# Optimization experiments

Hardware: AMD Instinct MI355X
Metric: run time of the kernel (lower is better)

The kernel has to match this reference:

```python
import jax, jax.numpy as jnp
import numpy as np

B, T, S = 4, 16, 4096
H, KV, D, DIM = 32, 8, 128, 4096
BASE = 10000.0
START = 2048
SCALE = 1.0 / np.sqrt(D)


def _rope(t, cos, sin):
    # t: [B, T, nh, D]; ggml 'normal' rope rotates adjacent pairs (x[2i], x[2i+1])
    b, tt, nh, d = t.shape
    t2 = t.reshape(b, tt, nh, d // 2, 2)
    x0, x1 = t2[..., 0], t2[..., 1]
    c = cos[None, :, None, :]  # [1, T, 1, D/2]
    s = sin[None, :, None, :]
    r = jnp.stack([x0 * c - x1 * s, x0 * s + x1 * c], axis=-1)
    return r.reshape(b, tt, nh, d)


def setup_inputs() -> dict:
    key = jax.random.key(0)
    ks = jax.random.split(key, 8)
    x = jax.random.normal(ks[0], (B, T, DIM), dtype=jnp.float32)
    k_cache = jax.random.normal(ks[1], (B, S, KV, D), dtype=jnp.float32)
    v_cache = jax.random.normal(ks[2], (B, S, KV, D), dtype=jnp.float32)
    wq = jax.random.normal(ks[3], (H * D, DIM), dtype=jnp.float32) * 0.02
    wk = jax.random.normal(ks[4], (KV * D, DIM), dtype=jnp.float32) * 0.02
    wv = jax.random.normal(ks[5], (KV * D, DIM), dtype=jnp.float32) * 0.02
    wo = jax.random.normal(ks[6], (DIM, H * D), dtype=jnp.float32) * 0.02
    input_pos = jnp.arange(T, dtype=jnp.int32) + START  # contiguous decode chunk
    inv_freq = BASE ** (-jnp.arange(0, D, 2, dtype=jnp.float32) / D)  # [D/2]
    ang = input_pos.astype(jnp.float32)[:, None] * inv_freq[None, :]  # [T, D/2]
    freqs_cos = jnp.cos(ang)
    freqs_sin = jnp.sin(ang)
    # causal mask: kv position <= query absolute position, [T, S] bool
    attn_mask = jnp.arange(S, dtype=jnp.int32)[None, :] <= input_pos[:, None]
    return {"x": x, "freqs_cos": freqs_cos, "freqs_sin": freqs_sin,
            "input_pos": input_pos, "attn_mask": attn_mask,
            "k_cache": k_cache, "v_cache": v_cache,
            "wq": wq, "wk": wk, "wv": wv, "wo": wo}


def reference(x, freqs_cos, freqs_sin, input_pos, attn_mask, k_cache, v_cache, wq, wk, wv, wo):
    b, t, _ = x.shape
    q = (x @ wq.T).reshape(b, t, H, D)
    k = (x @ wk.T).reshape(b, t, KV, D)
    v = (x @ wv.T).reshape(b, t, KV, D)
    q = _rope(q, freqs_cos, freqs_sin)
    k = _rope(k, freqs_cos, freqs_sin)
    # KV-cache scatter (index_copy_ along dim 1)
    kc = k_cache.at[:, input_pos].set(k)  # [B, S, KV, D]
    vc = v_cache.at[:, input_pos].set(v)
    g = H // KV
    qh = q.transpose(0, 2, 1, 3).reshape(b, KV, g, t, D)  # [B, KV, g, T, D]
    kf = kc.transpose(0, 2, 1, 3)  # [B, KV, S, D]
    vf = vc.transpose(0, 2, 1, 3)
    scores = jnp.einsum('bkgtd,bksd->bkgts', qh, kf) * SCALE
    scores = jnp.where(attn_mask[None, None, None], scores, jnp.finfo(scores.dtype).min)
    probs = jax.nn.softmax(scores, axis=-1)
    y = jnp.einsum('bkgts,bksd->bkgtd', probs, vf)  # [B, KV, g, T, D]
    y = y.reshape(b, H, t, D).transpose(0, 2, 1, 3).reshape(b, t, H * D)
    return y @ wo.T
```

## Files before the change

kernel.cpp:

```cpp
#include <hip/hip_runtime.h>


#define SCALE_F 0.08838834764831845f

typedef __attribute__((ext_vector_type(8))) short bf16x8;
typedef __attribute__((ext_vector_type(4))) float f32x4;

__device__ __forceinline__ unsigned short f2b(float f) {
    union { float f; unsigned u; } v; v.f = f;
    unsigned r = v.u + 0x7FFFu + ((v.u >> 16) & 1u);
    return (unsigned short)(r >> 16);
}

__device__ __forceinline__ bf16x8 pack8(float4 a, float4 b) {
    bf16x8 r;
    r[0] = (short)f2b(a.x); r[1] = (short)f2b(a.y); r[2] = (short)f2b(a.z); r[3] = (short)f2b(a.w);
    r[4] = (short)f2b(b.x); r[5] = (short)f2b(b.y); r[6] = (short)f2b(b.z); r[7] = (short)f2b(b.w);
    return r;
}

__global__ __launch_bounds__(256) void qkv_gemm_kernel(
    const float* __restrict__ x,
    const float* __restrict__ wq, const float* __restrict__ wk, const float* __restrict__ wvp,
    float* __restrict__ part)
{
    __shared__ unsigned short x_lds[64][72];
    __shared__ unsigned short w_lds[32][72];
    const int tid = threadIdx.x, lane = tid & 63, wid = tid >> 6;
    const int n0 = blockIdx.x * 32;
    const int split = blockIdx.y;
    const int k_base = split * 512;

    const float* wptr; int nn;
    if (n0 < 4096)      { wptr = wq;  nn = n0; }
    else if (n0 < 5120) { wptr = wk;  nn = n0 - 4096; }
    else                { wptr = wvp; nn = n0 - 5120; }

    const int xr = tid >> 2, xc = (tid & 3) * 16;
    const int wr = tid >> 3, wc = (tid & 7) * 8;
    const float* xp = x + xr * 4096 + k_base + xc;
    const float* wp = wptr + (nn + wr) * 4096 + k_base + wc;

    float4 rx0, rx1, rx2, rx3, rw0, rw1;
#define LOADQ(IT) do { const float* xq_ = xp + (IT) * 64; const float* wq_ = wp + (IT) * 64; \
    rx0 = *(const float4*)(xq_);      rx1 = *(const float4*)(xq_ + 4);  \
    rx2 = *(const float4*)(xq_ + 8);  rx3 = *(const float4*)(xq_ + 12); \
    rw0 = *(const float4*)(wq_);      rw1 = *(const float4*)(wq_ + 4); } while (0)

    f32x4 acc0 = {0.f,0.f,0.f,0.f}, acc1 = {0.f,0.f,0.f,0.f};
    LOADQ(0);
    for (int it = 0; it < 8; ++it) {
        *(bf16x8*)&x_lds[xr][xc]     = pack8(rx0, rx1);
        *(bf16x8*)&x_lds[xr][xc + 8] = pack8(rx2, rx3);
        *(bf16x8*)&w_lds[wr][wc]     = pack8(rw0, rw1);
        __syncthreads();
        if (it < 7) LOADQ(it + 1);
        #pragma unroll
        for (int kk = 0; kk < 2; ++kk) {
            bf16x8 a  = *(bf16x8*)&x_lds[16 * wid + (lane & 15)][kk * 32 + 8 * (lane >> 4)];
            bf16x8 b0 = *(bf16x8*)&w_lds[(lane & 15)][kk * 32 + 8 * (lane >> 4)];
            bf16x8 b1 = *(bf16x8*)&w_lds[16 + (lane & 15)][kk * 32 + 8 * (lane >> 4)];
            acc0 = __builtin_amdgcn_mfma_f32_16x16x32_bf16(a, b0, acc0, 0, 0, 0);
            acc1 = __builtin_amdgcn_mfma_f32_16x16x32_bf16(a, b1, acc1, 0, 0, 0);
        }
        __syncthreads();
    }
#undef LOADQ
    #pragma unroll
    for (int nt = 0; nt < 2; ++nt) {
        f32x4 acc = nt ? acc1 : acc0;
        #pragma unroll
        for (int r = 0; r < 4; ++r) {
            int row = 16 * wid + 4 * (lane >> 4) + r;
            part[(split * 64 + row) * 6144 + n0 + nt * 16 + (lane & 15)] = acc[r];
        }
    }
}

__global__ __launch_bounds__(256) void qkv_reduce_kernel(
    const float* __restrict__ part,
    const float* __restrict__ fcos, const float* __restrict__ fsin,
    unsigned short* __restrict__ q_out, unsigned short* __restrict__ k_new,
    unsigned short* __restrict__ v_new)
{
    const int gid = blockIdx.x * 256 + threadIdx.x;
    const int m = gid / 1536;
    const int n = (gid % 1536) * 4;
    float4 s = {0.f,0.f,0.f,0.f};
    #pragma unroll
    for (int sp = 0; sp < 8; ++sp) {
        float4 v = *(const float4*)(part + (size_t)(sp * 64 + m) * 6144 + n);
        s.x += v.x; s.y += v.y; s.z += v.z; s.w += v.w;
    }
    const int t = m & 15, b = m >> 4;
    ushort4 o;
    if (n < 5120) {
        int d = n & 127;
        float c0 = fcos[t * 64 + (d >> 1)],     s0 = fsin[t * 64 + (d >> 1)];
        float c1 = fcos[t * 64 + (d >> 1) + 1], s1 = fsin[t * 64 + (d >> 1) + 1];
        o.x = f2b(s.x * c0 - s.y * s0);
        o.y = f2b(s.x * s0 + s.y * c0);
        o.z = f2b(s.z * c1 - s.w * s1);
        o.w = f2b(s.z * s1 + s.w * c1);
    } else {
        o.x = f2b(s.x); o.y = f2b(s.y); o.z = f2b(s.z); o.w = f2b(s.w);
    }
    if (n < 4096) {
        int h = n >> 7, d = n & 127;
        int row = (b * 8 + (h >> 2)) * 64 + (h & 3) * 16 + t;
        *(ushort4*)(q_out + row * 128 + d) = o;
    } else if (n < 5120) {
        int idx = n - 4096, kvh = idx >> 7, d = idx & 127;
        *(ushort4*)(k_new + ((b * 8 + kvh) * 16 + t) * 128 + d) = o;
    } else {
        int idx = n - 5120, kvh = idx >> 7, d = idx & 127;
        *(ushort4*)(v_new + ((b * 8 + kvh) * 16 + t) * 128 + d) = o;
    }
}

__global__ __launch_bounds__(256) void attn_kernel(
    const float* __restrict__ k_cache, const float* __restrict__ v_cache,
    const unsigned short* __restrict__ q_glob,
    const unsigned short* __restrict__ k_new, const unsigned short* __restrict__ v_new,
    float* __restrict__ y_part, float* __restrict__ ml)
{
    __shared__ unsigned short smem[32256];
    unsigned short* kv_lds = smem;
    unsigned short* p_lds  = smem + 21504;

    const int bk = blockIdx.x >> 4;
    const int c  = blockIdx.x & 15;
    const int b = bk >> 3, kvh = bk & 7;
    const int tid = threadIdx.x, lane = tid & 63, wid = tid >> 6;
    const int s0 = c * 128;
    const bool last = (c == 15);

    bf16x8 aq[4];
    {
        const unsigned short* qp = q_glob + (bk * 64 + 16 * wid + (lane & 15)) * 128 + 8 * (lane >> 4);
        #pragma unroll
        for (int kk = 0; kk < 4; ++kk) aq[kk] = *(const bf16x8*)(qp + kk * 32);
    }

    const int rr = tid >> 5, ln4 = (tid & 31) * 4;
    {
        const float* kb = k_cache + ((size_t)(b * 4096 + s0) * 8 + kvh) * 128;
        #pragma unroll 4
        for (int it = 0; it < 16; ++it) {
            int srow = it * 8 + rr;
            float4 kf = *(const float4*)(kb + (size_t)srow * 1024 + ln4);
            ushort4 k4; k4.x = f2b(kf.x); k4.y = f2b(kf.y); k4.z = f2b(kf.z); k4.w = f2b(kf.w);
            *(ushort4*)&kv_lds[srow * 136 + ln4] = k4;
        }
        if (last) {
            int row = tid >> 4, c8 = (tid & 15) * 8;
            *(bf16x8*)&kv_lds[(128 + row) * 136 + c8] =
                *(const bf16x8*)(k_new + (bk * 16 + row) * 128 + c8);
        }
    }
    __syncthreads();

    f32x4 sc[9];
    f32x4 zero4 = {0.f,0.f,0.f,0.f};
    #pragma unroll
    for (int st = 0; st < 9; ++st) sc[st] = zero4;
    #pragma unroll
    for (int kk = 0; kk < 4; ++kk) {
        #pragma unroll
        for (int st = 0; st < 9; ++st) {
            if (st == 8 && !last) continue;
            bf16x8 bf = *(bf16x8*)&kv_lds[(st * 16 + (lane & 15)) * 136 + kk * 32 + 8 * (lane >> 4)];
            sc[st] = __builtin_amdgcn_mfma_f32_16x16x32_bf16(aq[kk], bf, sc[st], 0, 0, 0);
        }
    }

    float mrow[4], lrow[4];
    #pragma unroll
    for (int r = 0; r < 4; ++r) {
        int trow = 4 * (lane >> 4) + r;
        float mx = -3.0e38f;
        #pragma unroll
        for (int st = 0; st < 9; ++st) {
            if (st == 8 && !last) continue;
            float s = sc[st][r] * SCALE_F;
            if (st == 8 && (lane & 15) > trow) s = -3.0e38f;
            sc[st][r] = s;
            mx = fmaxf(mx, s);
        }
        mx = fmaxf(mx, __shfl_xor(mx, 1));
        mx = fmaxf(mx, __shfl_xor(mx, 2));
        mx = fmaxf(mx, __shfl_xor(mx, 4));
        mx = fmaxf(mx, __shfl_xor(mx, 8));
        float sum = 0.f;
        #pragma unroll
        for (int st = 0; st < 9; ++st) {
            if (st == 8 && !last) continue;
            float p = __expf(sc[st][r] - mx);
            sc[st][r] = p;
            sum += p;
        }
        sum += __shfl_xor(sum, 1);
        sum += __shfl_xor(sum, 2);
        sum += __shfl_xor(sum, 4);
        sum += __shfl_xor(sum, 8);
        mrow[r] = mx; lrow[r] = sum;
    }

    #pragma unroll
    for (int st = 0; st < 9; ++st) {
        if (st == 8 && !last) continue;
        #pragma unroll
        for (int r = 0; r < 4; ++r)
            p_lds[(16 * wid + 4 * (lane >> 4) + r) * 168 + st * 16 + (lane & 15)] = f2b(sc[st][r]);
    }
    if ((lane & 15) == 0) {
        #pragma unroll
        for (int r = 0; r < 4; ++r) {
            int row = 16 * wid + 4 * (lane >> 4) + r;
            ml[(bk * 16 + c) * 128 + row * 2 + 0] = mrow[r];
            ml[(bk * 16 + c) * 128 + row * 2 + 1] = lrow[r];
        }
    }
    __syncthreads();

    {
        const float* vb = v_cache + ((size_t)(b * 4096 + s0) * 8 + kvh) * 128;
        #pragma unroll 4
        for (int it = 0; it < 16; ++it) {
            int srow = it * 8 + rr;
            float4 vf = *(const float4*)(vb + (size_t)srow * 1024 + ln4);
            kv_lds[(ln4 + 0) * 168 + srow] = f2b(vf.x);
            kv_lds[(ln4 + 1) * 168 + srow] = f2b(vf.y);
            kv_lds[(ln4 + 2) * 168 + srow] = f2b(vf.z);
            kv_lds[(ln4 + 3) * 168 + srow] = f2b(vf.w);
        }
        if (last) {
            int row = tid >> 4, c8 = (tid & 15) * 8;
            bf16x8 vv = *(const bf16x8*)(v_new + (bk * 16 + row) * 128 + c8);
            #pragma unroll
            for (int u = 0; u < 8; ++u)
                kv_lds[(c8 + u) * 168 + 128 + row] = (unsigned short)vv[u];
            int pr = tid >> 2, pc = (tid & 3) * 4;
            #pragma unroll
            for (int u = 0; u < 4; ++u) p_lds[pr * 168 + 144 + pc + u] = 0;
            int vr = tid >> 1, vc = (tid & 1) * 8;
            #pragma unroll
            for (int u = 0; u < 8; ++u) kv_lds[vr * 168 + 144 + vc + u] = 0;
        }
    }
    __syncthreads();

    f32x4 o_[8];
    #pragma unroll
    for (int nt = 0; nt < 8; ++nt) o_[nt] = zero4;
    #pragma unroll
    for (int ks = 0; ks < 5; ++ks) {
        if (ks == 4 && !last) continue;
        bf16x8 a = *(bf16x8*)&p_lds[(16 * wid + (lane & 15)) * 168 + ks * 32 + 8 * (lane >> 4)];
        #pragma unroll
        for (int nt = 0; nt < 8; ++nt) {
            bf16x8 bf = *(bf16x8*)&kv_lds[(nt * 16 + (lane & 15)) * 168 + ks * 32 + 8 * (lane >> 4)];
            o_[nt] = __builtin_amdgcn_mfma_f32_16x16x32_bf16(a, bf, o_[nt], 0, 0, 0);
        }
    }
    float* yp = y_part + (size_t)(bk * 16 + c) * 8192;
    #pragma unroll
    for (int nt = 0; nt < 8; ++nt) {
        #pragma unroll
        for (int r = 0; r < 4; ++r)
            yp[(16 * wid + 4 * (lane >> 4) + r) * 128 + nt * 16 + (lane & 15)] = o_[nt][r];
    }
}

__global__ __launch_bounds__(256) void combine_kernel(
    const float* __restrict__ y_part, const float* __restrict__ ml,
    unsigned short* __restrict__ y_attn)
{
    const int bid = blockIdx.x;
    const int bk = bid >> 3, rg = bid & 7;
    const int b = bk >> 3, kvh = bk & 7;
    const int tid = threadIdx.x;
    const int d = tid & 127, r2 = tid >> 7;
    for (int rr = 0; rr < 8; rr += 2) {
        int row = rg * 8 + rr + r2;
        float mv[16], lv[16], M = -3.0e38f;
        #pragma unroll
        for (int cc = 0; cc < 16; ++cc) {
            mv[cc] = ml[(bk * 16 + cc) * 128 + row * 2 + 0];
            lv[cc] = ml[(bk * 16 + cc) * 128 + row * 2 + 1];
            M = fmaxf(M, mv[cc]);
        }
        float den = 0.f, acc = 0.f;
        #pragma unroll
        for (int cc = 0; cc < 16; ++cc) {
            float co = __expf(mv[cc] - M);
            den += co * lv[cc];
            acc += co * y_part[((size_t)(bk * 16 + cc) * 64 + row) * 128 + d];
        }
        float y = acc / den;
        int gi = row >> 4, t = row & 15;
        y_attn[(b * 16 + t) * 4096 + (kvh * 4 + gi) * 128 + d] = f2b(y);
    }
}

__global__ __launch_bounds__(256) void proj_gemm_kernel(
    const unsigned short* __restrict__ y_attn, const float* __restrict__ wo,
    float* __restrict__ part)
{
    __shared__ unsigned short a_lds[64][72];
    __shared__ unsigned short w_lds[32][72];
    const int tid = threadIdx.x, lane = tid & 63, wid = tid >> 6;
    const int n0 = blockIdx.x * 32;
    const int k_base = blockIdx.y * 512;

    const int ar = tid >> 2, ac = (tid & 3) * 16;
    const int wr = tid >> 3, wc = (tid & 7) * 8;
    const unsigned short* ap = y_attn + ar * 4096 + k_base + ac;
    const float* wp = wo + (n0 + wr) * 4096 + k_base + wc;

    bf16x8 ra0, ra1; float4 rw0, rw1;
#define LOADP(IT) do { const unsigned short* aq_ = ap + (IT) * 64; const float* wq_ = wp + (IT) * 64; \
    ra0 = *(const bf16x8*)(aq_); ra1 = *(const bf16x8*)(aq_ + 8); \
    rw0 = *(const float4*)(wq_); rw1 = *(const float4*)(wq_ + 4); } while (0)

    f32x4 acc0 = {0.f,0.f,0.f,0.f}, acc1 = {0.f,0.f,0.f,0.f};
    LOADP(0);
    for (int it = 0; it < 8; ++it) {
        *(bf16x8*)&a_lds[ar][ac]     = ra0;
        *(bf16x8*)&a_lds[ar][ac + 8] = ra1;
        *(bf16x8*)&w_lds[wr][wc]     = pack8(rw0, rw1);
        __syncthreads();
        if (it < 7) LOADP(it + 1);
        #pragma unroll
        for (int kk = 0; kk < 2; ++kk) {
            bf16x8 a  = *(bf16x8*)&a_lds[16 * wid + (lane & 15)][kk * 32 + 8 * (lane >> 4)];
            bf16x8 b0 = *(bf16x8*)&w_lds[(lane & 15)][kk * 32 + 8 * (lane >> 4)];
            bf16x8 b1 = *(bf16x8*)&w_lds[16 + (lane & 15)][kk * 32 + 8 * (lane >> 4)];
            acc0 = __builtin_amdgcn_mfma_f32_16x16x32_bf16(a, b0, acc0, 0, 0, 0);
            acc1 = __builtin_amdgcn_mfma_f32_16x16x32_bf16(a, b1, acc1, 0, 0, 0);
        }
        __syncthreads();
    }
#undef LOADP
    #pragma unroll
    for (int nt = 0; nt < 2; ++nt) {
        f32x4 acc = nt ? acc1 : acc0;
        #pragma unroll
        for (int r = 0; r < 4; ++r) {
            int row = 16 * wid + 4 * (lane >> 4) + r;
            part[(size_t)(blockIdx.y * 64 + row) * 4096 + n0 + nt * 16 + (lane & 15)] = acc[r];
        }
    }
}

__global__ __launch_bounds__(256) void proj_reduce_kernel(
    const float* __restrict__ part, float* __restrict__ out)
{
    const int gid = blockIdx.x * 256 + threadIdx.x;
    const int m = gid >> 10;
    const int n = (gid & 1023) * 4;
    float4 s = {0.f,0.f,0.f,0.f};
    #pragma unroll
    for (int sp = 0; sp < 8; ++sp) {
        float4 v = *(const float4*)(part + (size_t)(sp * 64 + m) * 4096 + n);
        s.x += v.x; s.y += v.y; s.z += v.z; s.w += v.w;
    }
    *(float4*)(out + (size_t)m * 4096 + n) = s;
}

extern "C" void kernel_launch(void* const* d_in, const int* in_sizes, int n_in,
                              void* d_out, int out_size, void* d_ws, size_t ws_size,
                              hipStream_t stream)
{
    const float* x       = (const float*)d_in[0];
    const float* fcos    = (const float*)d_in[1];
    const float* fsin    = (const float*)d_in[2];
    const float* k_cache = (const float*)d_in[5];
    const float* v_cache = (const float*)d_in[6];
    const float* wq      = (const float*)d_in[7];
    const float* wk      = (const float*)d_in[8];
    const float* wv      = (const float*)d_in[9];
    const float* wo      = (const float*)d_in[10];

    char* p = (char*)d_ws;
    unsigned short* q_out  = (unsigned short*)p; p += 4 * 8 * 64 * 128 * 2;
    unsigned short* k_new  = (unsigned short*)p; p += 4 * 8 * 16 * 128 * 2;
    unsigned short* v_new  = (unsigned short*)p; p += 4 * 8 * 16 * 128 * 2;
    unsigned short* y_attn = (unsigned short*)p; p += 64 * 4096 * 2;
    float* mlbuf  = (float*)p; p += 32 * 16 * 64 * 2 * 4;
    float* y_part = (float*)p; p += (size_t)32 * 16 * 64 * 128 * 4;
    float* bigbuf = (float*)p;

    qkv_gemm_kernel<<<dim3(192, 8), 256, 0, stream>>>(x, wq, wk, wv, bigbuf);
    qkv_reduce_kernel<<<384, 256, 0, stream>>>(bigbuf, fcos, fsin, q_out, k_new, v_new);
    attn_kernel<<<512, 256, 0, stream>>>(k_cache, v_cache, q_out, k_new, v_new, y_part, mlbuf);
    combine_kernel<<<256, 256, 0, stream>>>(y_part, mlbuf, y_attn);
    proj_gemm_kernel<<<dim3(128, 8), 256, 0, stream>>>(y_attn, wo, bigbuf);
    proj_reduce_kernel<<<256, 256, 0, stream>>>(bigbuf, (float*)d_out);
}
```

Measured before the change: 78.50 us.

## Restructure QKV and output GEMMs to stage activations once and stream weights directly into MFMA registers

Both skinny GEMMs now load the whole 64x256 activation slice into LDS once per block. Each wave then streams its own 32 weight rows straight from global memory into registers, using double-buffered prefetch, and feeds them as MFMA B operands. This removes the per-iteration LDS round-trip and barriers for weights and reuses each weight fragment across four M tiles. The split-K factor doubles from 8 to 16, so the reduce kernels sum more partials and the partial buffers grow. Weight loads per lane are less coalesced (stride across rows), which may cost bandwidth on this weight-bound workload.

```diff
diff --git a/kernel.cpp b/kernel.cpp
--- a/kernel.cpp
+++ b/kernel.cpp
@@ -24,57 +24,67 @@
     const float* __restrict__ wq, const float* __restrict__ wk, const float* __restrict__ wvp,
     float* __restrict__ part)
 {
-    __shared__ unsigned short x_lds[64][72];
-    __shared__ unsigned short w_lds[32][72];
+    __shared__ unsigned short a_lds[64][258];
     const int tid = threadIdx.x, lane = tid & 63, wid = tid >> 6;
-    const int n0 = blockIdx.x * 32;
-    const int split = blockIdx.y;
-    const int k_base = split * 512;
-
+    const int k_base = blockIdx.y * 256;
+
+    {
+        const int sr = tid >> 2, sq = tid & 3;
+        const float* xp = x + (size_t)sr * 4096 + k_base;
+        #pragma unroll
+        for (int j = 0; j < 8; ++j) {
+            int col = 32 * j + 8 * sq;
+            float4 p0 = *(const float4*)(xp + col);
+            float4 p1 = *(const float4*)(xp + col + 4);
+            *(bf16x8*)&a_lds[sr][col] = pack8(p0, p1);
+        }
+    }
+    __syncthreads();
+
+    const int n0 = blockIdx.x * 128 + wid * 32;
     const float* wptr; int nn;
     if (n0 < 4096)      { wptr = wq;  nn = n0; }
     else if (n0 < 5120) { wptr = wk;  nn = n0 - 4096; }
     else                { wptr = wvp; nn = n0 - 5120; }
 
-    const int xr = tid >> 2, xc = (tid & 3) * 16;
-    const int wr = tid >> 3, wc = (tid & 7) * 8;
-    const float* xp = x + xr * 4096 + k_base + xc;
-    const float* wp = wptr + (nn + wr) * 4096 + k_base + wc;
-
-    float4 rx0, rx1, rx2, rx3, rw0, rw1;
-#define LOADQ(IT) do { const float* xq_ = xp + (IT) * 64; const float* wq_ = wp + (IT) * 64; \
-    rx0 = *(const float4*)(xq_);      rx1 = *(const float4*)(xq_ + 4);  \
-    rx2 = *(const float4*)(xq_ + 8);  rx3 = *(const float4*)(xq_ + 12); \
-    rw0 = *(const float4*)(wq_);      rw1 = *(const float4*)(wq_ + 4); } while (0)
-
-    f32x4 acc0 = {0.f,0.f,0.f,0.f}, acc1 = {0.f,0.f,0.f,0.f};
-    LOADQ(0);
-    for (int it = 0; it < 8; ++it) {
-        *(bf16x8*)&x_lds[xr][xc]     = pack8(rx0, rx1);
-        *(bf16x8*)&x_lds[xr][xc + 8] = pack8(rx2, rx3);
-        *(bf16x8*)&w_lds[wr][wc]     = pack8(rw0, rw1);
-        __syncthreads();
-        if (it < 7) LOADQ(it + 1);
-        #pragma unroll
-        for (int kk = 0; kk < 2; ++kk) {
-            bf16x8 a  = *(bf16x8*)&x_lds[16 * wid + (lane & 15)][kk * 32 + 8 * (lane >> 4)];
-            bf16x8 b0 = *(bf16x8*)&w_lds[(lane & 15)][kk * 32 + 8 * (lane >> 4)];
-            bf16x8 b1 = *(bf16x8*)&w_lds[16 + (lane & 15)][kk * 32 + 8 * (lane >> 4)];
-            acc0 = __builtin_amdgcn_mfma_f32_16x16x32_bf16(a, b0, acc0, 0, 0, 0);
-            acc1 = __builtin_amdgcn_mfma_f32_16x16x32_bf16(a, b1, acc1, 0, 0, 0);
-        }
-        __syncthreads();
-    }
-#undef LOADQ
-    #pragma unroll
-    for (int nt = 0; nt < 2; ++nt) {
-        f32x4 acc = nt ? acc1 : acc0;
-        #pragma unroll
-        for (int r = 0; r < 4; ++r) {
-            int row = 16 * wid + 4 * (lane >> 4) + r;
-            part[(split * 64 + row) * 6144 + n0 + nt * 16 + (lane & 15)] = acc[r];
-        }
-    }
+    const int l15 = lane & 15, lh = lane >> 4;
+    const float* w0 = wptr + (size_t)(nn + l15) * 4096 + k_base + 8 * lh;
+    const float* w1 = w0 + 16 * 4096;
+
+    float4 buf0[4], buf1[4];
+#define ISSUE0(S) do { buf0[0]=*(const float4*)(w0+(S)*32); buf0[1]=*(const float4*)(w0+(S)*32+4); \
+                       buf0[2]=*(const float4*)(w1+(S)*32); buf0[3]=*(const float4*)(w1+(S)*32+4); } while(0)
+#define ISSUE1(S) do { buf1[0]=*(const float4*)(w0+(S)*32); buf1[1]=*(const float4*)(w0+(S)*32+4); \
+                       buf1[2]=*(const float4*)(w1+(S)*32); buf1[3]=*(const float4*)(w1+(S)*32+4); } while(0)
+
+    f32x4 acc[4][2];
+    #pragma unroll
+    for (int m = 0; m < 4; ++m) { acc[m][0] = (f32x4){0,0,0,0}; acc[m][1] = (f32x4){0,0,0,0}; }
+
+    ISSUE0(0); ISSUE1(1);
+    #pragma unroll
+    for (int s = 0; s < 8; ++s) {
+        bf16x8 b0, b1;
+        if ((s & 1) == 0) { b0 = pack8(buf0[0], buf0[1]); b1 = pack8(buf0[2], buf0[3]); if (s < 6) ISSUE0(s + 2); }
+        else              { b0 = pack8(buf1[0], buf1[1]); b1 = pack8(buf1[2], buf1[3]); if (s < 6) ISSUE1(s + 2); }
+        #pragma unroll
+        for (int m = 0; m < 4; ++m) {
+            bf16x8 a = *(bf16x8*)&a_lds[16 * m + l15][s * 32 + 8 * lh];
+            acc[m][0] = __builtin_amdgcn_mfma_f32_16x16x32_bf16(a, b0, acc[m][0], 0, 0, 0);
+            acc[m][1] = __builtin_amdgcn_mfma_f32_16x16x32_bf16(a, b1, acc[m][1], 0, 0, 0);
+        }
+    }
+#undef ISSUE0
+#undef ISSUE1
+
+    float* pp = part + (size_t)blockIdx.y * 64 * 6144;
+    #pragma unroll
+    for (int m = 0; m < 4; ++m)
+        #pragma unroll
+        for (int nh = 0; nh < 2; ++nh)
+            #pragma unroll
+            for (int r = 0; r < 4; ++r)
+                pp[(16 * m + 4 * lh + r) * 6144 + n0 + nh * 16 + l15] = acc[m][nh][r];
 }
 
 __global__ __launch_bounds__(256) void qkv_reduce_kernel(
@@ -88,7 +98,7 @@
     const int n = (gid % 1536) * 4;
     float4 s = {0.f,0.f,0.f,0.f};
     #pragma unroll
-    for (int sp = 0; sp < 8; ++sp) {
+    for (int sp = 0; sp < 16; ++sp) {
         float4 v = *(const float4*)(part + (size_t)(sp * 64 + m) * 6144 + n);
         s.x += v.x; s.y += v.y; s.z += v.z; s.w += v.w;
     }
@@ -307,50 +317,60 @@
     const unsigned short* __restrict__ y_attn, const float* __restrict__ wo,
     float* __restrict__ part)
 {
-    __shared__ unsigned short a_lds[64][72];
-    __shared__ unsigned short w_lds[32][72];
+    __shared__ unsigned short a_lds[64][258];
     const int tid = threadIdx.x, lane = tid & 63, wid = tid >> 6;
-    const int n0 = blockIdx.x * 32;
-    const int k_base = blockIdx.y * 512;
-
-    const int ar = tid >> 2, ac = (tid & 3) * 16;
-    const int wr = tid >> 3, wc = (tid & 7) * 8;
-    const unsigned short* ap = y_attn + ar * 4096 + k_base + ac;
-    const float* wp = wo + (n0 + wr) * 4096 + k_base + wc;
-
-    bf16x8 ra0, ra1; float4 rw0, rw1;
-#define LOADP(IT) do { const unsigned short* aq_ = ap + (IT) * 64; const float* wq_ = wp + (IT) * 64; \
-    ra0 = *(const bf16x8*)(aq_); ra1 = *(const bf16x8*)(aq_ + 8); \
-    rw0 = *(const float4*)(wq_); rw1 = *(const float4*)(wq_ + 4); } while (0)
-
-    f32x4 acc0 = {0.f,0.f,0.f,0.f}, acc1 = {0.f,0.f,0.f,0.f};
-    LOADP(0);
-    for (int it = 0; it < 8; ++it) {
-        *(bf16x8*)&a_lds[ar][ac]     = ra0;
-        *(bf16x8*)&a_lds[ar][ac + 8] = ra1;
-        *(bf16x8*)&w_lds[wr][wc]     = pack8(rw0, rw1);
-        __syncthreads();
-        if (it < 7) LOADP(it + 1);
-        #pragma unroll
-        for (int kk = 0; kk < 2; ++kk) {
-            bf16x8 a  = *(bf16x8*)&a_lds[16 * wid + (lane & 15)][kk * 32 + 8 * (lane >> 4)];
-            bf16x8 b0 = *(bf16x8*)&w_lds[(lane & 15)][kk * 32 + 8 * (lane >> 4)];
-            bf16x8 b1 = *(bf16x8*)&w_lds[16 + (lane & 15)][kk * 32 + 8 * (lane >> 4)];
-            acc0 = __builtin_amdgcn_mfma_f32_16x16x32_bf16(a, b0, acc0, 0, 0, 0);
-            acc1 = __builtin_amdgcn_mfma_f32_16x16x32_bf16(a, b1, acc1, 0, 0, 0);
-        }
-        __syncthreads();
-    }
-#undef LOADP
-    #pragma unroll
-    for (int nt = 0; nt < 2; ++nt) {
-        f32x4 acc = nt ? acc1 : acc0;
-        #pragma unroll
-        for (int r = 0; r < 4; ++r) {
-            int row = 16 * wid + 4 * (lane >> 4) + r;
-            part[(size_t)(blockIdx.y * 64 + row) * 4096 + n0 + nt * 16 + (lane & 15)] = acc[r];
-        }
-    }
+    const int k_base = blockIdx.y * 256;
+
+    {
+        const int sr = tid >> 2, sq = tid & 3;
+        const unsigned short* ap = y_attn + (size_t)sr * 4096 + k_base;
+        #pragma unroll
+        for (int j = 0; j < 8; ++j) {
+            int col = 32 * j + 8 * sq;
+            *(bf16x8*)&a_lds[sr][col] = *(const bf16x8*)(ap + col);
+        }
+    }
+    __syncthreads();
+
+    const int n0 = blockIdx.x * 128 + wid * 32;
+    const int l15 = lane & 15, lh = lane >> 4;
+    const float* w0 = wo + (size_t)(n0 + l15) * 4096 + k_base + 8 * lh;
+    const float* w1 = w0 + 16 * 4096;
+
+    float4 buf0[4], buf1[4];
+#define ISSUE0(S) do { buf0[0]=*(const float4*)(w0+(S)*32); buf0[1]=*(const float4*)(w0+(S)*32+4); \
+                       buf0[2]=*(const float4*)(w1+(S)*32); buf0[3]=*(const float4*)(w1+(S)*32+4); } while(0)
+#define ISSUE1(S) do { buf1[0]=*(const float4*)(w0+(S)*32); buf1[1]=*(const float4*)(w0+(S)*32+4); \
+                       buf1[2]=*(const float4*)(w1+(S)*32); buf1[3]=*(const float4*)(w1+(S)*32+4); } while(0)
+
+    f32x4 acc[4][2];
+    #pragma unroll
+    for (int m = 0; m < 4; ++m) { acc[m][0] = (f32x4){0,0,0,0}; acc[m][1] = (f32x4){0,0,0,0}; }
+
+    ISSUE0(0); ISSUE1(1);
+    #pragma unroll
+    for (int s = 0; s < 8; ++s) {
+        bf16x8 b0, b1;
+        if ((s & 1) == 0) { b0 = pack8(buf0[0], buf0[1]); b1 = pack8(buf0[2], buf0[3]); if (s < 6) ISSUE0(s + 2); }
+        else              { b0 = pack8(buf1[0], buf1[1]); b1 = pack8(buf1[2], buf1[3]); if (s < 6) ISSUE1(s + 2); }
+        #pragma unroll
+        for (int m = 0; m < 4; ++m) {
+            bf16x8 a = *(bf16x8*)&a_lds[16 * m + l15][s * 32 + 8 * lh];
+            acc[m][0] = __builtin_amdgcn_mfma_f32_16x16x32_bf16(a, b0, acc[m][0], 0, 0, 0);
+            acc[m][1] = __builtin_amdgcn_mfma_f32_16x16x32_bf16(a, b1, acc[m][1], 0, 0, 0);
+        }
+    }
+#undef ISSUE0
+#undef ISSUE1
+
+    float* pp = part + (size_t)blockIdx.y * 64 * 4096;
+    #pragma unroll
+    for (int m = 0; m < 4; ++m)
+        #pragma unroll
+        for (int nh = 0; nh < 2; ++nh)
+            #pragma unroll
+            for (int r = 0; r < 4; ++r)
+                pp[(16 * m + 4 * lh + r) * 4096 + n0 + nh * 16 + l15] = acc[m][nh][r];
 }
 
 __global__ __launch_bounds__(256) void proj_reduce_kernel(
@@ -361,7 +381,7 @@
     const int n = (gid & 1023) * 4;
     float4 s = {0.f,0.f,0.f,0.f};
     #pragma unroll
-    for (int sp = 0; sp < 8; ++sp) {
+    for (int sp = 0; sp < 16; ++sp) {
         float4 v = *(const float4*)(part + (size_t)(sp * 64 + m) * 4096 + n);
         s.x += v.x; s.y += v.y; s.z += v.z; s.w += v.w;
     }
@@ -391,10 +411,10 @@
     float* y_part = (float*)p; p += (size_t)32 * 16 * 64 * 128 * 4;
     float* bigbuf = (float*)p;
 
-    qkv_gemm_kernel<<<dim3(192, 8), 256, 0, stream>>>(x, wq, wk, wv, bigbuf);
+    qkv_gemm_kernel<<<dim3(48, 16), 256, 0, stream>>>(x, wq, wk, wv, bigbuf);
     qkv_reduce_kernel<<<384, 256, 0, stream>>>(bigbuf, fcos, fsin, q_out, k_new, v_new);
     attn_kernel<<<512, 256, 0, stream>>>(k_cache, v_cache, q_out, k_new, v_new, y_part, mlbuf);
     combine_kernel<<<256, 256, 0, stream>>>(y_part, mlbuf, y_attn);
-    proj_gemm_kernel<<<dim3(128, 8), 256, 0, stream>>>(y_attn, wo, bigbuf);
+    proj_gemm_kernel<<<dim3(32, 16), 256, 0, stream>>>(y_attn, wo, bigbuf);
     proj_reduce_kernel<<<256, 256, 0, stream>>>(bigbuf, (float*)d_out);
 }
```

Result: slower. 80.70 us (+2.8%).

## Stage GEMM tiles via direct global-to-LDS loads with double buffering and wider N tiles

Applied to the files above, without the earlier changes.

Both the QKV and output-projection GEMMs now copy fp32 (and bf16) tiles straight from global memory into swizzled, double-buffered LDS using global_load_lds. Conversion to bf16 happens when fragments are read from LDS instead of before the store. Each block also covers 64 output columns instead of 32, halving the grid, and the bf16 rounding helper switches to the library intrinsic. The aim is to overlap weight streaming with MFMA work and cut register round-trips, at the cost of more LDS per block, fewer blocks, and repeated pack work on every fragment read.

```diff
diff --git a/kernel.cpp b/kernel.cpp
--- a/kernel.cpp
+++ b/kernel.cpp
@@ -1,4 +1,5 @@
 #include <hip/hip_runtime.h>
+#include <hip/hip_bf16.h>
 
 
 #define SCALE_F 0.08838834764831845f
@@ -7,9 +8,8 @@
 typedef __attribute__((ext_vector_type(4))) float f32x4;
 
 __device__ __forceinline__ unsigned short f2b(float f) {
-    union { float f; unsigned u; } v; v.f = f;
-    unsigned r = v.u + 0x7FFFu + ((v.u >> 16) & 1u);
-    return (unsigned short)(r >> 16);
+    __hip_bfloat16 h = __float2bfloat16(f);
+    return *reinterpret_cast<unsigned short*>(&h);
 }
 
 __device__ __forceinline__ bf16x8 pack8(float4 a, float4 b) {
@@ -19,62 +19,74 @@
     return r;
 }
 
+__device__ __forceinline__ void gl_lds16(const void* g, void* l) {
+    __builtin_amdgcn_global_load_lds(
+        (const __attribute__((address_space(1))) void*)g,
+        (__attribute__((address_space(3))) void*)l, 16, 0, 0);
+}
+
 __global__ __launch_bounds__(256) void qkv_gemm_kernel(
     const float* __restrict__ x,
     const float* __restrict__ wq, const float* __restrict__ wk, const float* __restrict__ wvp,
     float* __restrict__ part)
 {
-    __shared__ unsigned short x_lds[64][72];
-    __shared__ unsigned short w_lds[32][72];
+    __shared__ float lds[2][4096];
     const int tid = threadIdx.x, lane = tid & 63, wid = tid >> 6;
-    const int n0 = blockIdx.x * 32;
-    const int split = blockIdx.y;
-    const int k_base = split * 512;
+    const int l15 = lane & 15, lh = lane >> 4;
+    const int n0 = blockIdx.x * 64;
+    const int k_base = blockIdx.y * 512;
 
     const float* wptr; int nn;
     if (n0 < 4096)      { wptr = wq;  nn = n0; }
     else if (n0 < 5120) { wptr = wk;  nn = n0 - 4096; }
     else                { wptr = wvp; nn = n0 - 5120; }
 
-    const int xr = tid >> 2, xc = (tid & 3) * 16;
-    const int wr = tid >> 3, wc = (tid & 7) * 8;
-    const float* xp = x + xr * 4096 + k_base + xc;
-    const float* wp = wptr + (nn + wr) * 4096 + k_base + wc;
-
-    float4 rx0, rx1, rx2, rx3, rw0, rw1;
-#define LOADQ(IT) do { const float* xq_ = xp + (IT) * 64; const float* wq_ = wp + (IT) * 64; \
-    rx0 = *(const float4*)(xq_);      rx1 = *(const float4*)(xq_ + 4);  \
-    rx2 = *(const float4*)(xq_ + 8);  rx3 = *(const float4*)(xq_ + 12); \
-    rw0 = *(const float4*)(wq_);      rw1 = *(const float4*)(wq_ + 4); } while (0)
-
-    f32x4 acc0 = {0.f,0.f,0.f,0.f}, acc1 = {0.f,0.f,0.f,0.f};
-    LOADQ(0);
-    for (int it = 0; it < 8; ++it) {
-        *(bf16x8*)&x_lds[xr][xc]     = pack8(rx0, rx1);
-        *(bf16x8*)&x_lds[xr][xc + 8] = pack8(rx2, rx3);
-        *(bf16x8*)&w_lds[wr][wc]     = pack8(rw0, rw1);
+    const int srow   = lane >> 3;
+    const int schunk = (lane & 7) ^ srow;
+    const float* gx0 = x    + (size_t)(16 * wid + srow) * 4096      + k_base + schunk * 4;
+    const float* gx1 = gx0  + (size_t)8 * 4096;
+    const float* gw0 = wptr + (size_t)(nn + 16 * wid + srow) * 4096 + k_base + schunk * 4;
+    const float* gw1 = gw0  + (size_t)8 * 4096;
+
+#define STAGE(BUF, T) do { const int off_ = (T) * 32; \
+    gl_lds16(gx0 + off_, &lds[BUF][(16 * wid) * 32]); \
+    gl_lds16(gx1 + off_, &lds[BUF][(16 * wid + 8) * 32]); \
+    gl_lds16(gw0 + off_, &lds[BUF][2048 + (16 * wid) * 32]); \
+    gl_lds16(gw1 + off_, &lds[BUF][2048 + (16 * wid + 8) * 32]); \
+} while (0)
+
+    const int c0off = ((2 * lh)     ^ (l15 & 7)) * 4;
+    const int c1off = ((2 * lh + 1) ^ (l15 & 7)) * 4;
+
+    f32x4 acc[4];
+    #pragma unroll
+    for (int nf = 0; nf < 4; ++nf) acc[nf] = (f32x4){0.f, 0.f, 0.f, 0.f};
+
+    STAGE(0, 0);
+    __syncthreads();
+    for (int t = 0; t < 16; ++t) {
+        const int buf = t & 1;
+        if (t < 15) STAGE(buf ^ 1, t + 1);
+        const float* xt = &lds[buf][0];
+        const float* wt = &lds[buf][2048];
+        const int ar = (16 * wid + l15) * 32;
+        bf16x8 a = pack8(*(const float4*)&xt[ar + c0off], *(const float4*)&xt[ar + c1off]);
+        #pragma unroll
+        for (int nf = 0; nf < 4; ++nf) {
+            const int br = (nf * 16 + l15) * 32;
+            bf16x8 b = pack8(*(const float4*)&wt[br + c0off], *(const float4*)&wt[br + c1off]);
+            acc[nf] = __builtin_amdgcn_mfma_f32_16x16x32_bf16(a, b, acc[nf], 0, 0, 0);
+        }
         __syncthreads();
-        if (it < 7) LOADQ(it + 1);
-        #pragma unroll
-        for (int kk = 0; kk < 2; ++kk) {
-            bf16x8 a  = *(bf16x8*)&x_lds[16 * wid + (lane & 15)][kk * 32 + 8 * (lane >> 4)];
-            bf16x8 b0 = *(bf16x8*)&w_lds[(lane & 15)][kk * 32 + 8 * (lane >> 4)];
-            bf16x8 b1 = *(bf16x8*)&w_lds[16 + (lane & 15)][kk * 32 + 8 * (lane >> 4)];
-            acc0 = __builtin_amdgcn_mfma_f32_16x16x32_bf16(a, b0, acc0, 0, 0, 0);
-            acc1 = __builtin_amdgcn_mfma_f32_16x16x32_bf16(a, b1, acc1, 0, 0, 0);
-        }
-        __syncthreads();
-    }
-#undef LOADQ
-    #pragma unroll
-    for (int nt = 0; nt < 2; ++nt) {
-        f32x4 acc = nt ? acc1 : acc0;
-        #pragma unroll
-        for (int r = 0; r < 4; ++r) {
-            int row = 16 * wid + 4 * (lane >> 4) + r;
-            part[(split * 64 + row) * 6144 + n0 + nt * 16 + (lane & 15)] = acc[r];
-        }
-    }
+    }
+#undef STAGE
+
+    float* pp = part + (size_t)blockIdx.y * 64 * 6144 + n0;
+    #pragma unroll
+    for (int nf = 0; nf < 4; ++nf)
+        #pragma unroll
+        for (int r = 0; r < 4; ++r)
+            pp[(16 * wid + 4 * lh + r) * 6144 + nf * 16 + l15] = acc[nf][r];
 }
 
 __global__ __launch_bounds__(256) void qkv_reduce_kernel(
@@ -307,50 +319,56 @@
     const unsigned short* __restrict__ y_attn, const float* __restrict__ wo,
     float* __restrict__ part)
 {
-    __shared__ unsigned short a_lds[64][72];
-    __shared__ unsigned short w_lds[32][72];
+    __shared__ float wlds[2][2048];
+    __shared__ unsigned short alds[2][2048];
     const int tid = threadIdx.x, lane = tid & 63, wid = tid >> 6;
-    const int n0 = blockIdx.x * 32;
+    const int l15 = lane & 15, lh = lane >> 4;
+    const int n0 = blockIdx.x * 64;
     const int k_base = blockIdx.y * 512;
 
-    const int ar = tid >> 2, ac = (tid & 3) * 16;
-    const int wr = tid >> 3, wc = (tid & 7) * 8;
-    const unsigned short* ap = y_attn + ar * 4096 + k_base + ac;
-    const float* wp = wo + (n0 + wr) * 4096 + k_base + wc;
-
-    bf16x8 ra0, ra1; float4 rw0, rw1;
-#define LOADP(IT) do { const unsigned short* aq_ = ap + (IT) * 64; const float* wq_ = wp + (IT) * 64; \
-    ra0 = *(const bf16x8*)(aq_); ra1 = *(const bf16x8*)(aq_ + 8); \
-    rw0 = *(const float4*)(wq_); rw1 = *(const float4*)(wq_ + 4); } while (0)
-
-    f32x4 acc0 = {0.f,0.f,0.f,0.f}, acc1 = {0.f,0.f,0.f,0.f};
-    LOADP(0);
-    for (int it = 0; it < 8; ++it) {
-        *(bf16x8*)&a_lds[ar][ac]     = ra0;
-        *(bf16x8*)&a_lds[ar][ac + 8] = ra1;
-        *(bf16x8*)&w_lds[wr][wc]     = pack8(rw0, rw1);
+    const int arow = lane >> 2, achk = lane & 3;
+    const unsigned short* ga = y_attn + (size_t)(16 * wid + arow) * 4096 + k_base + achk * 8;
+    const int srow   = lane >> 3;
+    const int schunk = (lane & 7) ^ srow;
+    const float* gw0 = wo + (size_t)(n0 + 16 * wid + srow) * 4096 + k_base + schunk * 4;
+    const float* gw1 = gw0 + (size_t)8 * 4096;
+
+#define STAGE(BUF, T) do { \
+    gl_lds16(ga + (T) * 32,       &alds[BUF][(16 * wid) * 32]); \
+    gl_lds16(gw0 + (T) * 32,      &wlds[BUF][(16 * wid) * 32]); \
+    gl_lds16(gw1 + (T) * 32,      &wlds[BUF][(16 * wid + 8) * 32]); \
+} while (0)
+
+    const int c0off = ((2 * lh)     ^ (l15 & 7)) * 4;
+    const int c1off = ((2 * lh + 1) ^ (l15 & 7)) * 4;
+
+    f32x4 acc[4];
+    #pragma unroll
+    for (int nf = 0; nf < 4; ++nf) acc[nf] = (f32x4){0.f, 0.f, 0.f, 0.f};
+
+    STAGE(0, 0);
+    __syncthreads();
+    for (int t = 0; t < 16; ++t) {
+        const int buf = t & 1;
+        if (t < 15) STAGE(buf ^ 1, t + 1);
+        bf16x8 a = *(const bf16x8*)&alds[buf][(16 * wid + l15) * 32 + lh * 8];
+        const float* wt = &wlds[buf][0];
+        #pragma unroll
+        for (int nf = 0; nf < 4; ++nf) {
+            const int br = (nf * 16 + l15) * 32;
+            bf16x8 b = pack8(*(const float4*)&wt[br + c0off], *(const float4*)&wt[br + c1off]);
+            acc[nf] = __builtin_amdgcn_mfma_f32_16x16x32_bf16(a, b, acc[nf], 0, 0, 0);
+        }
         __syncthreads();
-        if (it < 7) LOADP(it + 1);
-        #pragma unroll
-        for (int kk = 0; kk < 2; ++kk) {
-            bf16x8 a  = *(bf16x8*)&a_lds[16 * wid + (lane & 15)][kk * 32 + 8 * (lane >> 4)];
-            bf16x8 b0 = *(bf16x8*)&w_lds[(lane & 15)][kk * 32 + 8 * (lane >> 4)];
-            bf16x8 b1 = *(bf16x8*)&w_lds[16 + (lane & 15)][kk * 32 + 8 * (lane >> 4)];
-            acc0 = __builtin_amdgcn_mfma_f32_16x16x32_bf16(a, b0, acc0, 0, 0, 0);
-            acc1 = __builtin_amdgcn_mfma_f32_16x16x32_bf16(a, b1, acc1, 0, 0, 0);
-        }
-        __syncthreads();
-    }
-#undef LOADP
-    #pragma unroll
-    for (int nt = 0; nt < 2; ++nt) {
-        f32x4 acc = nt ? acc1 : acc0;
-        #pragma unroll
-        for (int r = 0; r < 4; ++r) {
-            int row = 16 * wid + 4 * (lane >> 4) + r;
-            part[(size_t)(blockIdx.y * 64 + row) * 4096 + n0 + nt * 16 + (lane & 15)] = acc[r];
-        }
-    }
+    }
+#undef STAGE
+
+    float* pp = part + (size_t)blockIdx.y * 64 * 4096 + n0;
+    #pragma unroll
+    for (int nf = 0; nf < 4; ++nf)
+        #pragma unroll
+        for (int r = 0; r < 4; ++r)
+            pp[(16 * wid + 4 * lh + r) * 4096 + nf * 16 + l15] = acc[nf][r];
 }
 
 __global__ __launch_bounds__(256) void proj_reduce_kernel(
@@ -391,10 +409,10 @@
     float* y_part = (float*)p; p += (size_t)32 * 16 * 64 * 128 * 4;
     float* bigbuf = (float*)p;
 
-    qkv_gemm_kernel<<<dim3(192, 8), 256, 0, stream>>>(x, wq, wk, wv, bigbuf);
+    qkv_gemm_kernel<<<dim3(96, 8), 256, 0, stream>>>(x, wq, wk, wv, bigbuf);
     qkv_reduce_kernel<<<384, 256, 0, stream>>>(bigbuf, fcos, fsin, q_out, k_new, v_new);
     attn_kernel<<<512, 256, 0, stream>>>(k_cache, v_cache, q_out, k_new, v_new, y_part, mlbuf);
     combine_kernel<<<256, 256, 0, stream>>>(y_part, mlbuf, y_attn);
-    proj_gemm_kernel<<<dim3(128, 8), 256, 0, stream>>>(y_attn, wo, bigbuf);
+    proj_gemm_kernel<<<dim3(64, 8), 256, 0, stream>>>(y_attn, wo, bigbuf);
     proj_reduce_kernel<<<256, 256, 0, stream>>>(bigbuf, (float*)d_out);
 }
```

New measurement: 80.67 us. +2.8%, slower.
